# Kernel optimization log

Measured on AMD Instinct MI355X. Metric: run time of the kernel, lower is better.

## Reference

```python
import jax, jax.numpy as jnp
import numpy as np

N, D, E = 50000, 128, 800000
BN_EPS = 1e-3  # keras BatchNormalization default


def _ffn_block(x, g, b, m, v, W, bias):
    # BatchNorm (inference) -> Dropout (identity at inference) -> Dense + exact GELU
    xn = (x - m) * g * jax.lax.rsqrt(v + BN_EPS) + b
    return jax.nn.gelu(xn @ W + bias, approximate=False)


def setup_inputs() -> dict:
    key = jax.random.key(0)
    ks = jax.random.split(key, 24)
    inp = {
        "node_reps": jax.random.normal(ks[0], (N, D), dtype=jnp.float32),
        "edges": jax.random.randint(ks[1], (2, E), 0, N, dtype=jnp.int32),
        "edge_weights": jax.random.uniform(ks[2], (E,), dtype=jnp.float32),
    }
    def bn(i, dim):
        return (jax.random.normal(ks[i], (dim,)) * 0.1 + 1.0,   # gamma
                jax.random.normal(ks[i + 1], (dim,)) * 0.1,      # beta
                jax.random.normal(ks[i + 2], (dim,)) * 0.1,      # moving mean
                jax.random.uniform(ks[i + 3], (dim,)) + 0.5)     # moving var (>0)
    # prepare FFN: two blocks, D->D then D->D
    inp["pre_bn1_g"], inp["pre_bn1_b"], inp["pre_bn1_m"], inp["pre_bn1_v"] = bn(3, D)
    inp["pre_w1"] = jax.random.normal(ks[7], (D, D)) * (1.0 / np.sqrt(D))
    inp["pre_b1"] = jnp.zeros((D,), jnp.float32)
    inp["pre_bn2_g"], inp["pre_bn2_b"], inp["pre_bn2_m"], inp["pre_bn2_v"] = bn(8, D)
    inp["pre_w2"] = jax.random.normal(ks[12], (D, D)) * (1.0 / np.sqrt(D))
    inp["pre_b2"] = jnp.zeros((D,), jnp.float32)
    # update FFN: concat -> 2D input, then D->D
    inp["upd_bn1_g"], inp["upd_bn1_b"], inp["upd_bn1_m"], inp["upd_bn1_v"] = bn(13, 2 * D)
    inp["upd_w1"] = jax.random.normal(ks[17], (2 * D, D)) * (1.0 / np.sqrt(2 * D))
    inp["upd_b1"] = jnp.zeros((D,), jnp.float32)
    inp["upd_bn2_g"], inp["upd_bn2_b"], inp["upd_bn2_m"], inp["upd_bn2_v"] = bn(18, D)
    inp["upd_w2"] = jax.random.normal(ks[22], (D, D)) * (1.0 / np.sqrt(D))
    inp["upd_b2"] = jnp.zeros((D,), jnp.float32)
    return inp


def reference(node_reps, edges, edge_weights,
              pre_bn1_g, pre_bn1_b, pre_bn1_m, pre_bn1_v, pre_w1, pre_b1,
              pre_bn2_g, pre_bn2_b, pre_bn2_m, pre_bn2_v, pre_w2, pre_b2,
              upd_bn1_g, upd_bn1_b, upd_bn1_m, upd_bn1_v, upd_w1, upd_b1,
              upd_bn2_g, upd_bn2_b, upd_bn2_m, upd_bn2_v, upd_w2, upd_b2):
    num_nodes = node_reps.shape[0]
    node_idx, nbr_idx = edges[0], edges[1]
    # gather neighbour representations [E, D]
    nbr = jnp.take(node_reps, nbr_idx, axis=0)
    # prepare: FFN then scale by edge weights
    msg = _ffn_block(nbr, pre_bn1_g, pre_bn1_b, pre_bn1_m, pre_bn1_v, pre_w1, pre_b1)
    msg = _ffn_block(msg, pre_bn2_g, pre_bn2_b, pre_bn2_m, pre_bn2_v, pre_w2, pre_b2)
    msg = msg * edge_weights[:, None]
    # aggregate: segment_sum scatter back to nodes [N, D]
    agg = jax.ops.segment_sum(msg, node_idx, num_segments=num_nodes)
    # update: concat + FFN, then L2 normalize
    h = jnp.concatenate([node_reps, agg], axis=-1)  # [N, 2D]
    out = _ffn_block(h, upd_bn1_g, upd_bn1_b, upd_bn1_m, upd_bn1_v, upd_w1, upd_b1)
    out = _ffn_block(out, upd_bn2_g, upd_bn2_b, upd_bn2_m, upd_bn2_v, upd_w2, upd_b2)
    out = out * jax.lax.rsqrt(jnp.maximum(jnp.sum(out * out, axis=-1, keepdims=True), 1e-12))
    return out
```

## Files before the change

### kernel.cpp

```cpp
#include <hip/hip_runtime.h>
#include <hip/hip_bf16.h>
#include <math.h>

#define NN 50000
#define DD 128
#define EE 800000

static constexpr float BN_EPS = 1e-3f;

typedef __attribute__((ext_vector_type(8))) short bf16x8;
typedef __attribute__((ext_vector_type(4))) float f32x4;

#define MFMA16(a, b, c) __builtin_amdgcn_mfma_f32_16x16x32_bf16((a), (b), (c), 0, 0, 0)

__device__ __forceinline__ float gelu_f(float x) {
    float ax = fabsf(x) * 0.7071067811865475f;
    float t = __builtin_amdgcn_rcpf(fmaf(0.3275911f, ax, 1.0f));
    float p = t * fmaf(t, fmaf(t, fmaf(t, fmaf(t, 1.061405429f, -1.453152027f),
                                       1.421413741f), -0.284496736f), 0.254829592f);
    float e = __expf(-ax * ax);
    float er = fmaf(-p, e, 1.0f);
    float s = copysignf(er, x);
    return 0.5f * x * (1.0f + s);
}

__device__ __forceinline__ ushort f2bf_rn(float f) {
    uint u = __float_as_uint(f);
    return (ushort)((u + 0x7FFFu + ((u >> 16) & 1u)) >> 16);
}
__device__ __forceinline__ float bf2f(ushort h) {
    return __uint_as_float(((uint)h) << 16);
}

__device__ __forceinline__ uint pk2(float a, float b) {
    __hip_bfloat162 t = __float22bfloat162_rn(make_float2(a, b));
    uint r;
    __builtin_memcpy(&r, &t, 4);
    return r;
}

__device__ __forceinline__ void cvt_hilo(float4 x0, float4 x1, bf16x8& h, bf16x8& l) {
    float f[8] = {x0.x, x0.y, x0.z, x0.w, x1.x, x1.y, x1.z, x1.w};
    union U { uint u[4]; bf16x8 v; } uh, ul;
    #pragma unroll
    for (int j = 0; j < 4; ++j) {
        uint p = pk2(f[2 * j], f[2 * j + 1]);
        uh.u[j] = p;
        float h0 = __uint_as_float(p << 16);
        float h1 = __uint_as_float(p & 0xFFFF0000u);
        ul.u[j] = pk2(f[2 * j] - h0, f[2 * j + 1] - h1);
    }
    h = uh.v;
    l = ul.v;
}

__device__ __forceinline__ void pack_one(const float* __restrict__ W, const float* __restrict__ g,
                                         const float* __restrict__ v, ushort* __restrict__ hi,
                                         ushort* __restrict__ lo, int K, int idx) {
    int k = idx >> 7, col = idx & 127;
    float s = g[k] * rsqrtf(v[k] + BN_EPS);
    float f = s * W[idx];
    int S = K >> 5;
    int st = k >> 5, gq = (k >> 3) & 3, j = k & 7;
    int c = col >> 4, ln = (gq << 4) | (col & 15);
    int o = ((c * S + st) * 64 + ln) * 8 + j;
    ushort hb = f2bf_rn(f);
    hi[o] = hb;
    lo[o] = f2bf_rn(f - bf2f(hb));
}

__global__ void pack_all(
    const float* __restrict__ w1, const float* __restrict__ g1, const float* __restrict__ v1,
    ushort* __restrict__ W1h, ushort* __restrict__ W1l,
    const float* __restrict__ w2, const float* __restrict__ g2, const float* __restrict__ v2,
    ushort* __restrict__ W2h, ushort* __restrict__ W2l,
    const float* __restrict__ u1, const float* __restrict__ g3, const float* __restrict__ v3,
    ushort* __restrict__ U1h, ushort* __restrict__ U1l,
    const float* __restrict__ u2, const float* __restrict__ g4, const float* __restrict__ v4,
    ushort* __restrict__ U2h, ushort* __restrict__ U2l)
{
    int idx = blockIdx.x * 256 + threadIdx.x;
    if (idx < 16384)       pack_one(w1, g1, v1, W1h, W1l, 128, idx);
    else if (idx < 32768)  pack_one(w2, g2, v2, W2h, W2l, 128, idx - 16384);
    else if (idx < 65536)  pack_one(u1, g3, v3, U1h, U1l, 256, idx - 32768);
    else                   pack_one(u2, g4, v4, U2h, U2l, 128, idx - 65536);
}

__global__ void init_bias(const float* __restrict__ b1, const float* __restrict__ b2,
                          const float* __restrict__ ub1, const float* __restrict__ ub2,
                          float* __restrict__ B1f, float* __restrict__ B2f,
                          float* __restrict__ C1f, float* __restrict__ C2f) {
    int t = threadIdx.x;
    B1f[t] = b1[t]; B2f[t] = b2[t]; C1f[t] = ub1[t]; C2f[t] = ub2[t];
}

__global__ __launch_bounds__(256) void fold_all(
    const float* __restrict__ w1, const float* __restrict__ g1, const float* __restrict__ b1,
    const float* __restrict__ m1, const float* __restrict__ v1, float* __restrict__ B1f,
    const float* __restrict__ w2, const float* __restrict__ g2, const float* __restrict__ b2,
    const float* __restrict__ m2, const float* __restrict__ v2, float* __restrict__ B2f,
    const float* __restrict__ u1, const float* __restrict__ g3, const float* __restrict__ b3,
    const float* __restrict__ m3, const float* __restrict__ v3, float* __restrict__ C1f,
    const float* __restrict__ u2, const float* __restrict__ g4, const float* __restrict__ b4,
    const float* __restrict__ m4, const float* __restrict__ v4, float* __restrict__ C2f,
    int* __restrict__ cnt, int* __restrict__ spillCnt)
{
    for (int i = blockIdx.x * 256 + threadIdx.x; i < NN + 1; i += 20 * 256) {
        if (i < NN) cnt[i] = 0; else spillCnt[0] = 0;
    }

    const int rs = blockIdx.x * 32;
    const float *W, *g, *bb, *m, *v;
    float* bf;
    int k0;
    if (rs < 128)      { W = w1; g = g1; bb = b1; m = m1; v = v1; bf = B1f; k0 = rs; }
    else if (rs < 256) { W = w2; g = g2; bb = b2; m = m2; v = v2; bf = B2f; k0 = rs - 128; }
    else if (rs < 512) { W = u1; g = g3; bb = b3; m = m3; v = v3; bf = C1f; k0 = rs - 256; }
    else               { W = u2; g = g4; bb = b4; m = m4; v = v4; bf = C2f; k0 = rs - 512; }

    const int t = threadIdx.x, j = t & 127, h = t >> 7;
    float acc = 0.f;
    #pragma unroll
    for (int kk = 0; kk < 16; ++kk) {
        int k = k0 + h * 16 + kk;
        float s = g[k] * rsqrtf(v[k] + BN_EPS);
        float tt = bb[k] - m[k] * s;
        acc = fmaf(tt, W[k * DD + j], acc);
    }
    __shared__ float S[256];
    S[t] = acc;
    __syncthreads();
    if (h == 0) atomicAdd(&bf[j], S[j] + S[128 + j]);
}

#define YLD 136
#define BCAP 56
#define SPILL_CAP 100000
#define NCHUNK 400
#define CHSZ (EE / NCHUNK)
#define PSZ 6250
#define FILLB (NCHUNK * 8)

__global__ __launch_bounds__(512, 4) void prep_fill(
    const float* __restrict__ reps, const int* __restrict__ edges,
    const ushort* __restrict__ W1h, const ushort* __restrict__ W1l, const float* __restrict__ B1,
    const ushort* __restrict__ W2h, const ushort* __restrict__ W2l, const float* __restrict__ B2,
    ushort* __restrict__ msgN,
    int* __restrict__ cnt, int* __restrict__ spillCnt,
    int* __restrict__ spill, int* __restrict__ bucket)
{
    __shared__ ushort Yh[128 * YLD];

    if (blockIdx.x < FILLB) {
        const int part = blockIdx.x & 7;
        const int ch   = blockIdx.x >> 3;
        const int lo = part * PSZ, hi2 = lo + PSZ;
        const int base = ch * CHSZ;
        for (int i = threadIdx.x; i < CHSZ; i += 512) {
            int e = base + i;
            int d = edges[e];
            if (d >= lo && d < hi2) {
                int s = atomicAdd(&cnt[d], 1);
                if (s < BCAP) bucket[d * BCAP + s] = e;
                else { int sl = atomicAdd(spillCnt, 1); if (sl < SPILL_CAP) spill[sl] = e; }
            }
        }
        return;
    }

    const int pb = blockIdx.x - FILLB;
    if (pb >= 391) return;
    const int t = threadIdx.x;
    const int w = t >> 6, l = t & 63, lg = l >> 4, lr = l & 15;
    const int n0 = pb * 128;
    int n = n0 + w * 16 + lr;
    int nc = n < NN ? n : NN - 1;
    const float* src = reps + (size_t)nc * DD;

    float b1v[8], b2v[8];
    #pragma unroll
    for (int c = 0; c < 8; ++c) { b1v[c] = B1[c * 16 + lr]; b2v[c] = B2[c * 16 + lr]; }

    f32x4 acc[8];
    #pragma unroll
    for (int c = 0; c < 8; ++c) acc[c] = (f32x4)(0.f);

    #pragma unroll
    for (int s = 0; s < 4; ++s) {
        float4 x0 = *reinterpret_cast<const float4*>(src + s * 32 + lg * 8);
        float4 x1 = *reinterpret_cast<const float4*>(src + s * 32 + lg * 8 + 4);
        bf16x8 ah, al;
        cvt_hilo(x0, x1, ah, al);
        #pragma unroll
        for (int c = 0; c < 8; ++c) {
            bf16x8 bh = *reinterpret_cast<const bf16x8*>(W1h + (size_t)((c * 4 + s) * 64 + l) * 8);
            bf16x8 bl = *reinterpret_cast<const bf16x8*>(W1l + (size_t)((c * 4 + s) * 64 + l) * 8);
            acc[c] = MFMA16(al, bh, acc[c]);
            acc[c] = MFMA16(ah, bl, acc[c]);
            acc[c] = MFMA16(ah, bh, acc[c]);
        }
    }
    #pragma unroll
    for (int c = 0; c < 8; ++c) {
        #pragma unroll
        for (int i = 0; i < 4; ++i) {
            float yv = gelu_f(acc[c][i] + b1v[c]);
            Yh[(w * 16 + lg * 4 + i) * YLD + c * 16 + lr] = f2bf_rn(yv);
        }
    }

    #pragma unroll
    for (int c = 0; c < 8; ++c) acc[c] = (f32x4)(0.f);
    const ushort* yr = Yh + (w * 16 + lr) * YLD;
    #pragma unroll
    for (int s = 0; s < 4; ++s) {
        bf16x8 ah = *reinterpret_cast<const bf16x8*>(yr + s * 32 + lg * 8);
        #pragma unroll
        for (int c = 0; c < 8; ++c) {
            bf16x8 bh = *reinterpret_cast<const bf16x8*>(W2h + (size_t)((c * 4 + s) * 64 + l) * 8);
            bf16x8 bl = *reinterpret_cast<const bf16x8*>(W2l + (size_t)((c * 4 + s) * 64 + l) * 8);
            acc[c] = MFMA16(ah, bl, acc[c]);
            acc[c] = MFMA16(ah, bh, acc[c]);
        }
    }

    const int nrow = n0 + w * 16 + lg * 4;
    #pragma unroll
    for (int i = 0; i < 4; ++i) {
        if (nrow + i < NN) {
            #pragma unroll
            for (int c = 0; c < 8; ++c)
                msgN[(size_t)(nrow + i) * DD + c * 16 + lr] = f2bf_rn(gelu_f(acc[c][i] + b2v[c]));
        }
    }
}

__global__ __launch_bounds__(256, 8) void agg_node(
    const float* __restrict__ reps, const int* __restrict__ edges, const float* __restrict__ ew,
    const int* __restrict__ bucket, const int* __restrict__ cnt,
    const int* __restrict__ spillCnt, const int* __restrict__ spill,
    const ushort* __restrict__ msgN,
    const ushort* __restrict__ U1h, const ushort* __restrict__ U1l, const float* __restrict__ C1,
    const ushort* __restrict__ U2h, const ushort* __restrict__ U2l, const float* __restrict__ C2,
    float* __restrict__ out)
{
    __shared__ ushort aggL[16 * YLD];
    __shared__ ushort Yh[16 * YLD];
    __shared__ float ssqP[4][16];
    const int t = threadIdx.x;
    const int n0 = blockIdx.x * 16;

    {
        const int g = t >> 4, la = t & 15;
        const int node = n0 + g;
        const ushort* base = msgN + la * 8;
        float acc[8] = {0.f, 0.f, 0.f, 0.f, 0.f, 0.f, 0.f, 0.f};
        const int dc = cnt[node];
        const int deg = dc < BCAP ? dc : BCAP;
        const int* b = bucket + node * BCAP;
        int k = 0;
        for (; k + 3 < deg; k += 4) {
            int e0 = b[k], e1 = b[k + 1], e2 = b[k + 2], e3 = b[k + 3];
            int q0 = edges[EE + e0], q1 = edges[EE + e1];
            int q2 = edges[EE + e2], q3 = edges[EE + e3];
            float w0 = ew[e0], w1 = ew[e1], w2 = ew[e2], w3 = ew[e3];
            bf16x8 m0 = *reinterpret_cast<const bf16x8*>(base + (size_t)q0 * DD);
            bf16x8 m1 = *reinterpret_cast<const bf16x8*>(base + (size_t)q1 * DD);
            bf16x8 m2 = *reinterpret_cast<const bf16x8*>(base + (size_t)q2 * DD);
            bf16x8 m3 = *reinterpret_cast<const bf16x8*>(base + (size_t)q3 * DD);
            #pragma unroll
            for (int j = 0; j < 8; ++j) {
                acc[j] = fmaf(w0, bf2f((ushort)m0[j]), acc[j]);
                acc[j] = fmaf(w1, bf2f((ushort)m1[j]), acc[j]);
                acc[j] = fmaf(w2, bf2f((ushort)m2[j]), acc[j]);
                acc[j] = fmaf(w3, bf2f((ushort)m3[j]), acc[j]);
            }
        }
        for (; k < deg; ++k) {
            int e0 = b[k];
            int q0 = edges[EE + e0];
            float w0 = ew[e0];
            bf16x8 m0 = *reinterpret_cast<const bf16x8*>(base + (size_t)q0 * DD);
            #pragma unroll
            for (int j = 0; j < 8; ++j) acc[j] = fmaf(w0, bf2f((ushort)m0[j]), acc[j]);
        }
        if (dc > BCAP) {
            int sc = spillCnt[0]; if (sc > SPILL_CAP) sc = SPILL_CAP;
            for (int i = 0; i < sc; ++i) {
                int eid = spill[i];
                if (edges[eid] == node) {
                    int q0 = edges[EE + eid];
                    float w0 = ew[eid];
                    bf16x8 m0 = *reinterpret_cast<const bf16x8*>(base + (size_t)q0 * DD);
                    #pragma unroll
                    for (int j = 0; j < 8; ++j)
                        acc[j] = fmaf(w0, bf2f((ushort)m0[j]), acc[j]);
                }
            }
        }
        uint4 o;
        o.x = pk2(acc[0], acc[1]);
        o.y = pk2(acc[2], acc[3]);
        o.z = pk2(acc[4], acc[5]);
        o.w = pk2(acc[6], acc[7]);
        *reinterpret_cast<uint4*>(&aggL[g * YLD + la * 8]) = o;
    }
    __syncthreads();

    const int w = t >> 6, l = t & 63, lg = l >> 4, lr = l & 15;

    float c1v[2], c2v[2];
    #pragma unroll
    for (int cc = 0; cc < 2; ++cc) {
        c1v[cc] = C1[(2 * w + cc) * 16 + lr];
        c2v[cc] = C2[(2 * w + cc) * 16 + lr];
    }

    f32x4 acc[2];
    #pragma unroll
    for (int cc = 0; cc < 2; ++cc) acc[cc] = (f32x4)(0.f);

    #pragma unroll
    for (int s = 0; s < 4; ++s) {
        const float* sp = reps + (size_t)(n0 + lr) * DD + s * 32 + lg * 8;
        float4 x0 = *reinterpret_cast<const float4*>(sp);
        float4 x1 = *reinterpret_cast<const float4*>(sp + 4);
        bf16x8 ah, al;
        cvt_hilo(x0, x1, ah, al);
        #pragma unroll
        for (int cc = 0; cc < 2; ++cc) {
            int c = 2 * w + cc;
            bf16x8 bh = *reinterpret_cast<const bf16x8*>(U1h + (size_t)((c * 8 + s) * 64 + l) * 8);
            bf16x8 bl = *reinterpret_cast<const bf16x8*>(U1l + (size_t)((c * 8 + s) * 64 + l) * 8);
            acc[cc] = MFMA16(al, bh, acc[cc]);
            acc[cc] = MFMA16(ah, bl, acc[cc]);
            acc[cc] = MFMA16(ah, bh, acc[cc]);
        }
    }
    const ushort* ar = aggL + lr * YLD;
    #pragma unroll
    for (int s = 4; s < 8; ++s) {
        bf16x8 ah = *reinterpret_cast<const bf16x8*>(ar + (s - 4) * 32 + lg * 8);
        #pragma unroll
        for (int cc = 0; cc < 2; ++cc) {
            int c = 2 * w + cc;
            bf16x8 bh = *reinterpret_cast<const bf16x8*>(U1h + (size_t)((c * 8 + s) * 64 + l) * 8);
            bf16x8 bl = *reinterpret_cast<const bf16x8*>(U1l + (size_t)((c * 8 + s) * 64 + l) * 8);
            acc[cc] = MFMA16(ah, bl, acc[cc]);
            acc[cc] = MFMA16(ah, bh, acc[cc]);
        }
    }
    #pragma unroll
    for (int cc = 0; cc < 2; ++cc) {
        #pragma unroll
        for (int i = 0; i < 4; ++i) {
            float yv = gelu_f(acc[cc][i] + c1v[cc]);
            Yh[(lg * 4 + i) * YLD + (2 * w + cc) * 16 + lr] = f2bf_rn(yv);
        }
    }
    __syncthreads();

    #pragma unroll
    for (int cc = 0; cc < 2; ++cc) acc[cc] = (f32x4)(0.f);
    const ushort* yr2 = Yh + lr * YLD;
    #pragma unroll
    for (int s = 0; s < 4; ++s) {
        bf16x8 ah = *reinterpret_cast<const bf16x8*>(yr2 + s * 32 + lg * 8);
        #pragma unroll
        for (int cc = 0; cc < 2; ++cc) {
            int c = 2 * w + cc;
            bf16x8 bh = *reinterpret_cast<const bf16x8*>(U2h + (size_t)((c * 4 + s) * 64 + l) * 8);
            bf16x8 bl = *reinterpret_cast<const bf16x8*>(U2l + (size_t)((c * 4 + s) * 64 + l) * 8);
            acc[cc] = MFMA16(ah, bl, acc[cc]);
            acc[cc] = MFMA16(ah, bh, acc[cc]);
        }
    }

    float ssq[4] = {0.f, 0.f, 0.f, 0.f};
    #pragma unroll
    for (int cc = 0; cc < 2; ++cc) {
        #pragma unroll
        for (int i = 0; i < 4; ++i) {
            float vv = gelu_f(acc[cc][i] + c2v[cc]);
            acc[cc][i] = vv;
            ssq[i] = fmaf(vv, vv, ssq[i]);
        }
    }
    #pragma unroll
    for (int i = 0; i < 4; ++i) {
        #pragma unroll
        for (int msk = 1; msk < 16; msk <<= 1) ssq[i] += __shfl_xor(ssq[i], msk);
    }
    const int row0 = lg * 4;
    if (lr == 0) {
        #pragma unroll
        for (int i = 0; i < 4; ++i) ssqP[w][row0 + i] = ssq[i];
    }
    __syncthreads();
    #pragma unroll
    for (int i = 0; i < 4; ++i) {
        float tot = ssqP[0][row0 + i] + ssqP[1][row0 + i] +
                    ssqP[2][row0 + i] + ssqP[3][row0 + i];
        float sc = rsqrtf(fmaxf(tot, 1e-12f));
        #pragma unroll
        for (int cc = 0; cc < 2; ++cc)
            out[(size_t)(n0 + row0 + i) * DD + (2 * w + cc) * 16 + lr] = acc[cc][i] * sc;
    }
}

extern "C" void kernel_launch(void* const* d_in, const int* in_sizes, int n_in,
                              void* d_out, int out_size, void* d_ws, size_t ws_size,
                              hipStream_t stream)
{
    const float* reps = (const float*)d_in[0];
    const int*   edges = (const int*)d_in[1];
    const float* ew   = (const float*)d_in[2];
    const float* bn1g = (const float*)d_in[3];
    const float* bn1b = (const float*)d_in[4];
    const float* bn1m = (const float*)d_in[5];
    const float* bn1v = (const float*)d_in[6];
    const float* w1   = (const float*)d_in[7];
    const float* b1   = (const float*)d_in[8];
    const float* bn2g = (const float*)d_in[9];
    const float* bn2b = (const float*)d_in[10];
    const float* bn2m = (const float*)d_in[11];
    const float* bn2v = (const float*)d_in[12];
    const float* w2   = (const float*)d_in[13];
    const float* b2   = (const float*)d_in[14];
    const float* ubn1g = (const float*)d_in[15];
    const float* ubn1b = (const float*)d_in[16];
    const float* ubn1m = (const float*)d_in[17];
    const float* ubn1v = (const float*)d_in[18];
    const float* u1    = (const float*)d_in[19];
    const float* ub1   = (const float*)d_in[20];
    const float* ubn2g = (const float*)d_in[21];
    const float* ubn2b = (const float*)d_in[22];
    const float* ubn2m = (const float*)d_in[23];
    const float* ubn2v = (const float*)d_in[24];
    const float* u2    = (const float*)d_in[25];
    const float* ub2   = (const float*)d_in[26];

    char* wsb = (char*)d_ws;
    ushort* msgN     = (ushort*)wsb;
    int*    bucket   = (int*)(wsb + 12800000);
    int*    cnt      = (int*)(wsb + 24000000);
    int*    spillCnt = (int*)(wsb + 24200000);
    int*    spill    = (int*)(wsb + 24200016);
    float*  B1f      = (float*)(wsb + 24600016);
    float*  B2f = B1f + 128;
    float*  C1f = B2f + 128;
    float*  C2f = C1f + 128;
    ushort* up  = (ushort*)(C2f + 128);
    ushort* W1h = up;
    ushort* W1l = W1h + 16384;
    ushort* W2h = W1l + 16384;
    ushort* W2l = W2h + 16384;
    ushort* U1h = W2l + 16384;
    ushort* U1l = U1h + 32768;
    ushort* U2h = U1l + 32768;
    ushort* U2l = U2h + 16384;
    if (ws_size < 24950000) return;

    init_bias<<<1, 128, 0, stream>>>(b1, b2, ub1, ub2, B1f, B2f, C1f, C2f);
    pack_all<<<320, 256, 0, stream>>>(w1, bn1g, bn1v, W1h, W1l,
                                      w2, bn2g, bn2v, W2h, W2l,
                                      u1, ubn1g, ubn1v, U1h, U1l,
                                      u2, ubn2g, ubn2v, U2h, U2l);
    fold_all<<<20, 256, 0, stream>>>(w1, bn1g, bn1b, bn1m, bn1v, B1f,
                                     w2, bn2g, bn2b, bn2m, bn2v, B2f,
                                     u1, ubn1g, ubn1b, ubn1m, ubn1v, C1f,
                                     u2, ubn2g, ubn2b, ubn2m, ubn2v, C2f,
                                     cnt, spillCnt);

    prep_fill<<<FILLB + 392, 512, 0, stream>>>(reps, edges, W1h, W1l, B1f,
                                               W2h, W2l, B2f, msgN,
                                               cnt, spillCnt, spill, bucket);
    agg_node<<<NN / 16, 256, 0, stream>>>(reps, edges, ew, bucket, cnt,
                                          spillCnt, spill, msgN,
                                          U1h, U1l, C1f, U2h, U2l, C2f,
                                          (float*)d_out);
}
```

Baseline: 155.8 us.

## Partition per-node edge buckets into four source-node sections

Each destination bucket is split into four sub-buckets keyed by source-node range, each holding up to 12 edges, with a counter per section. The aggregation then walks the sections in order, so gathers from msgN are grouped by source range, which may improve cache locality. The cost is a second edge read during fill, four times as many counters, and overflow into the slow spill path whenever one section exceeds 12 edges. The spill path scans the entire spill list, so it can trigger more often than with a single 56-entry bucket. The inner loop is also unrolled by 2 instead of 4.

```diff
diff --git a/kernel.cpp b/kernel.cpp
--- a/kernel.cpp
+++ b/kernel.cpp
@@ -103,10 +103,10 @@
     const float* __restrict__ m3, const float* __restrict__ v3, float* __restrict__ C1f,
     const float* __restrict__ u2, const float* __restrict__ g4, const float* __restrict__ b4,
     const float* __restrict__ m4, const float* __restrict__ v4, float* __restrict__ C2f,
-    int* __restrict__ cnt, int* __restrict__ spillCnt)
+    int* __restrict__ cnt4, int* __restrict__ spillCnt)
 {
-    for (int i = blockIdx.x * 256 + threadIdx.x; i < NN + 1; i += 20 * 256) {
-        if (i < NN) cnt[i] = 0; else spillCnt[0] = 0;
+    for (int i = blockIdx.x * 256 + threadIdx.x; i < NN * 4 + 1; i += 20 * 256) {
+        if (i < NN * 4) cnt4[i] = 0; else spillCnt[0] = 0;
     }
 
     const int rs = blockIdx.x * 32;
@@ -134,7 +134,10 @@
 }
 
 #define YLD 136
-#define BCAP 56
+#define SECN 4
+#define SECSZ 12500
+#define SEC_CAP 12
+#define BSTR (SECN * SEC_CAP)
 #define SPILL_CAP 100000
 #define NCHUNK 400
 #define CHSZ (EE / NCHUNK)
@@ -146,7 +149,7 @@
     const ushort* __restrict__ W1h, const ushort* __restrict__ W1l, const float* __restrict__ B1,
     const ushort* __restrict__ W2h, const ushort* __restrict__ W2l, const float* __restrict__ B2,
     ushort* __restrict__ msgN,
-    int* __restrict__ cnt, int* __restrict__ spillCnt,
+    int* __restrict__ cnt4, int* __restrict__ spillCnt,
     int* __restrict__ spill, int* __restrict__ bucket)
 {
     __shared__ ushort Yh[128 * YLD];
@@ -160,8 +163,10 @@
             int e = base + i;
             int d = edges[e];
             if (d >= lo && d < hi2) {
-                int s = atomicAdd(&cnt[d], 1);
-                if (s < BCAP) bucket[d * BCAP + s] = e;
+                int nb = edges[EE + e];
+                int sec = nb / SECSZ;
+                int s = atomicAdd(&cnt4[d * SECN + sec], 1);
+                if (s < SEC_CAP) bucket[d * BSTR + sec * SEC_CAP + s] = e;
                 else { int sl = atomicAdd(spillCnt, 1); if (sl < SPILL_CAP) spill[sl] = e; }
             }
         }
@@ -237,7 +242,7 @@
 
 __global__ __launch_bounds__(256, 8) void agg_node(
     const float* __restrict__ reps, const int* __restrict__ edges, const float* __restrict__ ew,
-    const int* __restrict__ bucket, const int* __restrict__ cnt,
+    const int* __restrict__ bucket, const int* __restrict__ cnt4,
     const int* __restrict__ spillCnt, const int* __restrict__ spill,
     const ushort* __restrict__ msgN,
     const ushort* __restrict__ U1h, const ushort* __restrict__ U1l, const float* __restrict__ C1,
@@ -255,36 +260,38 @@
         const int node = n0 + g;
         const ushort* base = msgN + la * 8;
         float acc[8] = {0.f, 0.f, 0.f, 0.f, 0.f, 0.f, 0.f, 0.f};
-        const int dc = cnt[node];
-        const int deg = dc < BCAP ? dc : BCAP;
-        const int* b = bucket + node * BCAP;
-        int k = 0;
-        for (; k + 3 < deg; k += 4) {
-            int e0 = b[k], e1 = b[k + 1], e2 = b[k + 2], e3 = b[k + 3];
-            int q0 = edges[EE + e0], q1 = edges[EE + e1];
-            int q2 = edges[EE + e2], q3 = edges[EE + e3];
-            float w0 = ew[e0], w1 = ew[e1], w2 = ew[e2], w3 = ew[e3];
-            bf16x8 m0 = *reinterpret_cast<const bf16x8*>(base + (size_t)q0 * DD);
-            bf16x8 m1 = *reinterpret_cast<const bf16x8*>(base + (size_t)q1 * DD);
-            bf16x8 m2 = *reinterpret_cast<const bf16x8*>(base + (size_t)q2 * DD);
-            bf16x8 m3 = *reinterpret_cast<const bf16x8*>(base + (size_t)q3 * DD);
-            #pragma unroll
-            for (int j = 0; j < 8; ++j) {
-                acc[j] = fmaf(w0, bf2f((ushort)m0[j]), acc[j]);
-                acc[j] = fmaf(w1, bf2f((ushort)m1[j]), acc[j]);
-                acc[j] = fmaf(w2, bf2f((ushort)m2[j]), acc[j]);
-                acc[j] = fmaf(w3, bf2f((ushort)m3[j]), acc[j]);
+        int4 c4 = *reinterpret_cast<const int4*>(&cnt4[node * SECN]);
+        const int cv[4] = {c4.x, c4.y, c4.z, c4.w};
+        bool hasSpill = (cv[0] > SEC_CAP) | (cv[1] > SEC_CAP) |
+                        (cv[2] > SEC_CAP) | (cv[3] > SEC_CAP);
+        const int* b = bucket + node * BSTR;
+        #pragma unroll
+        for (int sec = 0; sec < SECN; ++sec) {
+            int sc = cv[sec] < SEC_CAP ? cv[sec] : SEC_CAP;
+            const int* bs = b + sec * SEC_CAP;
+            int k = 0;
+            for (; k + 1 < sc; k += 2) {
+                int e0 = bs[k], e1 = bs[k + 1];
+                int q0 = edges[EE + e0], q1 = edges[EE + e1];
+                float w0 = ew[e0], w1 = ew[e1];
+                bf16x8 m0 = *reinterpret_cast<const bf16x8*>(base + (size_t)q0 * DD);
+                bf16x8 m1 = *reinterpret_cast<const bf16x8*>(base + (size_t)q1 * DD);
+                #pragma unroll
+                for (int j = 0; j < 8; ++j) {
+                    acc[j] = fmaf(w0, bf2f((ushort)m0[j]), acc[j]);
+                    acc[j] = fmaf(w1, bf2f((ushort)m1[j]), acc[j]);
+                }
             }
-        }
-        for (; k < deg; ++k) {
-            int e0 = b[k];
-            int q0 = edges[EE + e0];
-            float w0 = ew[e0];
-            bf16x8 m0 = *reinterpret_cast<const bf16x8*>(base + (size_t)q0 * DD);
-            #pragma unroll
-            for (int j = 0; j < 8; ++j) acc[j] = fmaf(w0, bf2f((ushort)m0[j]), acc[j]);
-        }
-        if (dc > BCAP) {
+            if (k < sc) {
+                int e0 = bs[k];
+                int q0 = edges[EE + e0];
+                float w0 = ew[e0];
+                bf16x8 m0 = *reinterpret_cast<const bf16x8*>(base + (size_t)q0 * DD);
+                #pragma unroll
+                for (int j = 0; j < 8; ++j) acc[j] = fmaf(w0, bf2f((ushort)m0[j]), acc[j]);
+            }
+        }
+        if (hasSpill) {
             int sc = spillCnt[0]; if (sc > SPILL_CAP) sc = SPILL_CAP;
             for (int i = 0; i < sc; ++i) {
                 int eid = spill[i];
@@ -443,10 +450,10 @@
     char* wsb = (char*)d_ws;
     ushort* msgN     = (ushort*)wsb;
     int*    bucket   = (int*)(wsb + 12800000);
-    int*    cnt      = (int*)(wsb + 24000000);
-    int*    spillCnt = (int*)(wsb + 24200000);
-    int*    spill    = (int*)(wsb + 24200016);
-    float*  B1f      = (float*)(wsb + 24600016);
+    int*    cnt4     = (int*)(wsb + 22400000);
+    int*    spillCnt = (int*)(wsb + 23200000);
+    int*    spill    = (int*)(wsb + 23200016);
+    float*  B1f      = (float*)(wsb + 23600016);
     float*  B2f = B1f + 128;
     float*  C1f = B2f + 128;
     float*  C2f = C1f + 128;
@@ -459,7 +466,7 @@
     ushort* U1l = U1h + 32768;
     ushort* U2h = U1l + 32768;
     ushort* U2l = U2h + 16384;
-    if (ws_size < 24950000) return;
+    if (ws_size < 23950000) return;
 
     init_bias<<<1, 128, 0, stream>>>(b1, b2, ub1, ub2, B1f, B2f, C1f, C2f);
     pack_all<<<320, 256, 0, stream>>>(w1, bn1g, bn1v, W1h, W1l,
@@ -470,12 +477,12 @@
                                      w2, bn2g, bn2b, bn2m, bn2v, B2f,
                                      u1, ubn1g, ubn1b, ubn1m, ubn1v, C1f,
                                      u2, ubn2g, ubn2b, ubn2m, ubn2v, C2f,
-                                     cnt, spillCnt);
+                                     cnt4, spillCnt);
 
     prep_fill<<<FILLB + 392, 512, 0, stream>>>(reps, edges, W1h, W1l, B1f,
                                                W2h, W2l, B2f, msgN,
-                                               cnt, spillCnt, spill, bucket);
-    agg_node<<<NN / 16, 256, 0, stream>>>(reps, edges, ew, bucket, cnt,
+                                               cnt4, spillCnt, spill, bucket);
+    agg_node<<<NN / 16, 256, 0, stream>>>(reps, edges, ew, bucket, cnt4,
                                           spillCnt, spill, msgN,
                                           U1h, U1l, C1f, U2h, U2l, C2f,
                                           (float*)d_out);
```

Measured after the change: 175.3 us. +12.6%, slower.
